# Performance work log

Hardware: AMD Instinct MI355X
Metric: run time of the kernel (lower is better)

Reference implementation:

```python
import jax, jax.numpy as jnp
import numpy as np

# Static configuration (matches init_kwargs)
B, C, H, W = 8, 64, 256, 256
WS = 8            # window size
HEADS = 4
DH = 16           # dim per head, HEADS*DH == C
L = WS * WS       # tokens per window
EPS_LN = 1e-5

# --- Swin relative-position index (static, numpy) ---
_coords = np.stack(np.meshgrid(np.arange(WS), np.arange(WS), indexing='ij'))  # [2,ws,ws]
_flat = _coords.reshape(2, -1)                                                # [2,L]
_rel = (_flat[:, :, None] - _flat[:, None, :]).transpose(1, 2, 0).copy()      # [L,L,2]
_rel[..., 0] += WS - 1
_rel[..., 1] += WS - 1
_rel[..., 0] *= 2 * WS - 1
REL_IDX = _rel.sum(-1)  # [L,L] ints in [0, (2ws-1)^2)


def _biasfree_ln(x, w):
    # x: [B,C,H,W]; BiasFree_LayerNorm over channel dim (biased var, no mean subtraction in scale)
    var = jnp.var(x, axis=1, keepdims=True)
    return x * jax.lax.rsqrt(var + EPS_LN) * w[None, :, None, None]


def _win_partition(t):  # [B,H,W,C] -> [N, L, C]
    t = t.reshape(B, H // WS, WS, W // WS, WS, C).transpose(0, 1, 3, 2, 4, 5)
    return t.reshape(-1, L, C)


def _win_reverse(t):  # [N, L, C] -> [B,H,W,C]
    t = t.reshape(B, H // WS, W // WS, WS, WS, C).transpose(0, 1, 3, 2, 4, 5)
    return t.reshape(B, H, W, C)


def _l2norm(t):
    # torch F.normalize(dim=-1) semantics
    n = jnp.sqrt(jnp.sum(t * t, axis=-1, keepdims=True))
    return t / jnp.maximum(n, 1e-12)


def _forward(x, illu_fea, ln1_w, ln2_w, w_qkv, b_qkv, rpb_table, w_proj, b_proj,
             temperature, w_qkv_m, w_dw, w_out_m):
    # ---------- spatial (window) attention branch ----------
    xs = _biasfree_ln(x, ln1_w).transpose(0, 2, 3, 1)          # [B,H,W,C]
    xw = _win_partition(xs)                                     # [N,L,C]
    iw = _win_partition(illu_fea.transpose(0, 2, 3, 1))         # [N,L,C]
    iw = iw.reshape(-1, L, HEADS, DH).transpose(0, 2, 1, 3)     # [N,h,L,d]

    qkv = (xw @ w_qkv + b_qkv).reshape(-1, L, 3, HEADS, DH).transpose(2, 0, 3, 1, 4)
    q, k, v = qkv[0], qkv[1], qkv[2]                            # [N,h,L,d]
    scale = DH ** (-0.5)
    attn = jnp.einsum('nhld,nhmd->nhlm', q * scale, k)          # [N,h,L,L]
    bias = rpb_table[REL_IDX.reshape(-1)].reshape(L, L, HEADS).transpose(2, 0, 1)
    attn = jax.nn.softmax(attn + bias[None], axis=-1)
    v = v * iw                                                  # illumination modulation
    out = jnp.einsum('nhlm,nhmd->nhld', attn, v)
    out = out.transpose(0, 2, 1, 3).reshape(-1, L, C) @ w_proj + b_proj
    win_out = _win_reverse(out).transpose(0, 3, 1, 2)           # [B,C,H,W]

    # ---------- channel (MDTA) attention branch ----------
    xm = _biasfree_ln(x, ln2_w)
    qkv_m = jnp.einsum('oc,bchw->bohw', w_qkv_m, xm)            # 1x1 conv, [B,3C,H,W]
    qkv_m = jax.lax.conv_general_dilated(
        qkv_m, w_dw, (1, 1), 'SAME', feature_group_count=3 * C,
        dimension_numbers=('NCHW', 'OIHW', 'NCHW'))             # depthwise 3x3
    qm, km, vm = jnp.split(qkv_m, 3, axis=1)                    # [B,C,H,W] each

    def heads(t):
        return t.reshape(B, HEADS, DH, H * W)                   # b (n d) h w -> b n d (hw)
    qm, km, vm, im = heads(qm), heads(km), heads(vm), heads(illu_fea)
    qm = _l2norm(qm)
    km = _l2norm(km)
    attn_c = jnp.einsum('bndx,bnex->bnde', qm, km) * temperature[None]  # [B,h,d,d]
    attn_c = jax.nn.softmax(attn_c, axis=-1)
    vm = vm * im                                                # illumination modulation
    out_c = jnp.einsum('bnde,bnex->bndx', attn_c, vm).reshape(B, C, H, W)
    mdta_out = jnp.einsum('oc,bchw->bohw', w_out_m, out_c)

    return x + win_out + mdta_out


def setup_inputs() -> dict:
    key = jax.random.key(0)
    ks = jax.random.split(key, 10)
    f32 = jnp.float32
    return {
        'x': jax.random.normal(ks[0], (B, C, H, W), f32),
        'illu_fea': jax.random.uniform(ks[1], (B, C, H, W), f32),
        'ln1_w': jnp.ones((C,), f32),
        'ln2_w': jnp.ones((C,), f32),
        'w_qkv': jax.random.normal(ks[2], (C, 3 * C), f32) * 0.02,
        'b_qkv': jnp.zeros((3 * C,), f32),
        'rpb_table': jax.random.normal(ks[3], ((2 * WS - 1) ** 2, HEADS), f32) * 0.02,
        'w_proj': jax.random.normal(ks[4], (C, C), f32) * 0.02,
        'b_proj': jnp.zeros((C,), f32),
        'temperature': jnp.ones((HEADS, 1, 1), f32),
        'w_qkv_m': jax.random.normal(ks[5], (3 * C, C), f32) * 0.02,
        'w_dw': jax.random.normal(ks[6], (3 * C, 1, 3, 3), f32) * 0.1,
        'w_out_m': jax.random.normal(ks[7], (C, C), f32) * 0.02,
    }


def reference(x, illu_fea, ln1_w, ln2_w, w_qkv, b_qkv, rpb_table, w_proj, b_proj,
              temperature, w_qkv_m, w_dw, w_out_m):
    return _forward(x, illu_fea, ln1_w, ln2_w, w_qkv, b_qkv, rpb_table, w_proj,
                    b_proj, temperature, w_qkv_m, w_dw, w_out_m)
```

## Files before the change

kernel.cpp:

```cpp
#include <hip/hip_runtime.h>
#include <hip/hip_bf16.h>

#define HW 65536
#define WIDTH 256
#define SP_OFF 77856768ull

typedef __attribute__((ext_vector_type(8))) short short8v;
typedef __attribute__((ext_vector_type(4))) short short4v;
typedef __attribute__((ext_vector_type(4))) float f32x4;

__device__ inline float bf2f(unsigned short u) {
  unsigned int i = ((unsigned int)u) << 16;
  float f; __builtin_memcpy(&f, &i, 4); return f;
}
__device__ inline unsigned short f2bf(float x) {
  __hip_bfloat16 h = __float2bfloat16(x);
  unsigned short u; __builtin_memcpy(&u, &h, 2); return u;
}

#define XH_IDX(p, g) ((p)*64 + ((((g) ^ ((p)&7)))<<3))
#define QC_IDX(ch, px) ((ch)*256 + ((((px)>>3) ^ ((ch)&7))<<3) + ((px)&7))
#define QCG_IDX(ch, G) ((ch)*256 + ((((G) ^ ((ch)&7)))<<3))

__global__ __launch_bounds__(256, 3) void k_spatial(
    const float* __restrict__ x, const float* __restrict__ illu,
    const float* __restrict__ ln1w, const float* __restrict__ wqkv,
    const float* __restrict__ bqkv, const float* __restrict__ rpb,
    const float* __restrict__ wproj, const float* __restrict__ bproj,
    float* __restrict__ out, unsigned short* __restrict__ sp, int use_sp)
{
  __shared__ __align__(16) unsigned short shbuf[9216];
  __shared__ __align__(16) unsigned short ks[64*72];
  __shared__ __align__(16) unsigned short vs[64*72];
  __shared__ __align__(16) unsigned short vsT[64*72];
  __shared__ float rpbs[900];
  __shared__ float rs_tok[64];

  unsigned short* xw = shbuf;
  unsigned short* qs = shbuf + 4608;

  const int tid = threadIdx.x;
  const int b = blockIdx.x & 7;
  const int grp = blockIdx.x >> 3;
  const float* xb = x + (size_t)b * 64 * HW;
  const float* ib = illu + (size_t)b * 64 * HW;

  const int lane = tid & 63;
  const int w = tid >> 6;
  const int fr = lane & 15;
  const int fg = lane >> 4;
  const int hb = w * 16;

  for (int i = tid; i < 900; i += 256) rpbs[i] = rpb[i];

  short8v bfq[3][2];
  float biasr[3];
  #pragma unroll
  for (int part = 0; part < 3; ++part) {
    int o = part * 64 + hb + fr;
    biasr[part] = bqkv[o];
    #pragma unroll
    for (int kh = 0; kh < 2; ++kh)
      #pragma unroll
      for (int j = 0; j < 8; ++j) {
        int c = kh * 32 + fg * 8 + j;
        bfq[part][kh][j] = (short)f2bf(wqkv[c * 192 + o] * ln1w[c]);
      }
  }
  short8v bfp[2];
  #pragma unroll
  for (int kh = 0; kh < 2; ++kh)
    #pragma unroll
    for (int j = 0; j < 8; ++j) {
      int c = kh * 32 + fg * 8 + j;
      bfp[kh][j] = (short)f2bf(wproj[c * 64 + hb + fr]);
    }

  for (int wi = 0; wi < 4; ++wi) {
    const int win = (grp << 2) + wi;
    const int h0 = (win >> 5) << 3;
    const int w0 = (win & 31) << 3;

    for (int i = tid; i < 1024; i += 256) {
      int c = i >> 4, seg = i & 15;
      int row = seg >> 1, half = (seg & 1) * 4;
      float4 v4 = *(const float4*)&xb[(size_t)c * HW + (h0 + row) * WIDTH + w0 + half];
      int p = row * 8 + half;
      xw[(p+0)*72 + c] = f2bf(v4.x);
      xw[(p+1)*72 + c] = f2bf(v4.y);
      xw[(p+2)*72 + c] = f2bf(v4.z);
      xw[(p+3)*72 + c] = f2bf(v4.w);
    }
    __syncthreads();
    {
      int l = tid >> 2, q4 = tid & 3;
      short8v v8a = *(const short8v*)&xw[l*72 + q4*16];
      short8v v8b = *(const short8v*)&xw[l*72 + q4*16 + 8];
      float s = 0.f, s2 = 0.f;
      #pragma unroll
      for (int j = 0; j < 8; ++j) {
        float va = bf2f((unsigned short)v8a[j]), vb = bf2f((unsigned short)v8b[j]);
        s += va + vb; s2 += va * va + vb * vb;
      }
      s += __shfl_down(s, 1); s2 += __shfl_down(s2, 1);
      s += __shfl_down(s, 2); s2 += __shfl_down(s2, 2);
      if (q4 == 0) {
        float mean = s * 0.015625f;
        float var = s2 * 0.015625f - mean * mean;
        rs_tok[l] = rsqrtf(var + 1e-5f);
      }
    }
    __syncthreads();
    {
      short8v a[4][2];
      #pragma unroll
      for (int rt = 0; rt < 4; ++rt)
        #pragma unroll
        for (int kh = 0; kh < 2; ++kh)
          a[rt][kh] = *(const short8v*)&xw[(rt*16 + fr)*72 + kh*32 + fg*8];
      #pragma unroll
      for (int part = 0; part < 3; ++part) {
        float bias = biasr[part];
        #pragma unroll
        for (int rt = 0; rt < 4; ++rt) {
          f32x4 acc = {0.f, 0.f, 0.f, 0.f};
          acc = __builtin_amdgcn_mfma_f32_16x16x32_bf16(a[rt][0], bfq[part][0], acc, 0, 0, 0);
          acc = __builtin_amdgcn_mfma_f32_16x16x32_bf16(a[rt][1], bfq[part][1], acc, 0, 0, 0);
          #pragma unroll
          for (int r = 0; r < 4; ++r) {
            int t = rt*16 + fg*4 + r;
            float val = acc[r] * rs_tok[t] + bias;
            if (part == 0)      qs[t*72 + hb + fr] = f2bf(val * 0.25f);
            else if (part == 1) ks[t*72 + hb + fr] = f2bf(val);
            else                vs[t*72 + hb + fr] = f2bf(val);
          }
        }
      }
    }
    __syncthreads();
    for (int i = tid; i < 1024; i += 256) {
      int c = i >> 4, seg = i & 15;
      int row = seg >> 1, half = (seg & 1) * 4;
      float4 v4 = *(const float4*)&ib[(size_t)c * HW + (h0 + row) * WIDTH + w0 + half];
      int p = row * 8 + half;
      xw[(p+0)*72 + c] = f2bf(v4.x);
      xw[(p+1)*72 + c] = f2bf(v4.y);
      xw[(p+2)*72 + c] = f2bf(v4.z);
      xw[(p+3)*72 + c] = f2bf(v4.w);
    }
    __syncthreads();
    for (int i = tid; i < 4096; i += 256) {
      int l = i >> 6, c = i & 63;
      unsigned short vb16 = f2bf(bf2f(vs[l*72 + c]) * bf2f(xw[l*72 + c]));
      vs[l*72 + c] = vb16;
      vsT[c*72 + ((((l >> 3) ^ (c & 7)) << 3) | (l & 7))] = vb16;
    }
    __syncthreads();
    float inv_s[4];
    {
      short8v zero8 = {0,0,0,0,0,0,0,0};
      short8v kf[4], qf[4];
      #pragma unroll
      for (int t = 0; t < 4; ++t) {
        if (fg < 2) {
          kf[t] = *(const short8v*)&ks[(t*16 + fr)*72 + hb + fg*8];
          qf[t] = *(const short8v*)&qs[(t*16 + fr)*72 + hb + fg*8];
        } else { kf[t] = zero8; qf[t] = zero8; }
      }
      f32x4 st[4][4];
      #pragma unroll
      for (int kt = 0; kt < 4; ++kt)
        #pragma unroll
        for (int qt = 0; qt < 4; ++qt) {
          f32x4 z = {0.f, 0.f, 0.f, 0.f};
          st[kt][qt] = __builtin_amdgcn_mfma_f32_16x16x32_bf16(kf[kt], qf[qt], z, 0, 0, 0);
        }
      float sc[4][16];
      #pragma unroll
      for (int qt = 0; qt < 4; ++qt) {
        int qi = qt*2 + (fr >> 3);
        int qj = fr & 7;
        float mx = -1e30f;
        #pragma unroll
        for (int kt = 0; kt < 4; ++kt) {
          int ki = kt*2 + (fg >> 1);
          int kj0 = (fg & 1) * 4;
          int base = ((qi - ki + 7)*15 + (qj - kj0 + 7))*4 + w;
          #pragma unroll
          for (int r = 0; r < 4; ++r) {
            float v = st[kt][qt][r] + rpbs[base - 4*r];
            sc[qt][kt*4 + r] = v;
            mx = fmaxf(mx, v);
          }
        }
        mx = fmaxf(mx, __shfl_xor(mx, 16));
        mx = fmaxf(mx, __shfl_xor(mx, 32));
        float ss = 0.f;
        #pragma unroll
        for (int j = 0; j < 16; ++j) { float e = __expf(sc[qt][j] - mx); sc[qt][j] = e; ss += e; }
        ss += __shfl_xor(ss, 16);
        ss += __shfl_xor(ss, 32);
        inv_s[qt] = 1.f / ss;
      }
      __syncthreads();
      unsigned short* pb = shbuf + w * 2304;
      f32x4 ot[4];
      #pragma unroll
      for (int nt = 0; nt < 4; ++nt) { f32x4 z = {0.f,0.f,0.f,0.f}; ot[nt] = z; }
      #pragma unroll
      for (int P = 0; P < 2; ++P) {
        #pragma unroll
        for (int qt = 0; qt < 4; ++qt)
          #pragma unroll
          for (int k2 = 0; k2 < 2; ++k2) {
            int kt = 2*P + k2;
            unsigned int lo = (unsigned)f2bf(sc[qt][kt*4+0]) | ((unsigned)f2bf(sc[qt][kt*4+1]) << 16);
            unsigned int hi = (unsigned)f2bf(sc[qt][kt*4+2]) | ((unsigned)f2bf(sc[qt][kt*4+3]) << 16);
            uint2 pk; pk.x = lo; pk.y = hi;
            *(uint2*)&pb[(qt*16 + fr)*36 + k2*16 + fg*4] = pk;
          }
        __syncthreads();
        short8v av = *(const short8v*)&vsT[(hb + fr)*72 + (((P*4 + fg) ^ ((hb + fr) & 7)) << 3)];
        #pragma unroll
        for (int nt = 0; nt < 4; ++nt) {
          short4v p0 = *(const short4v*)&pb[(nt*16 + fr)*36 + fg*8];
          short4v p1 = *(const short4v*)&pb[(nt*16 + fr)*36 + fg*8 + 4];
          short8v bv;
          #pragma unroll
          for (int j = 0; j < 4; ++j) { bv[j] = p0[j]; bv[4+j] = p1[j]; }
          ot[nt] = __builtin_amdgcn_mfma_f32_16x16x32_bf16(av, bv, ot[nt], 0, 0, 0);
        }
        __syncthreads();
      }
      #pragma unroll
      for (int nt = 0; nt < 4; ++nt) {
        float iv = inv_s[nt];
        unsigned int lo = (unsigned)f2bf(ot[nt][0]*iv) | ((unsigned)f2bf(ot[nt][1]*iv) << 16);
        unsigned int hi = (unsigned)f2bf(ot[nt][2]*iv) | ((unsigned)f2bf(ot[nt][3]*iv) << 16);
        uint2 pk; pk.x = lo; pk.y = hi;
        *(uint2*)&ks[(nt*16 + fr)*72 + hb + fg*4] = pk;
      }
    }
    __syncthreads();
    {
      short8v a[4][2];
      #pragma unroll
      for (int rt = 0; rt < 4; ++rt)
        #pragma unroll
        for (int kh = 0; kh < 2; ++kh)
          a[rt][kh] = *(const short8v*)&ks[(rt*16 + fr)*72 + kh*32 + fg*8];
      #pragma unroll
      for (int rt = 0; rt < 4; ++rt) {
        f32x4 acc = {0.f, 0.f, 0.f, 0.f};
        acc = __builtin_amdgcn_mfma_f32_16x16x32_bf16(a[rt][0], bfp[0], acc, 0, 0, 0);
        acc = __builtin_amdgcn_mfma_f32_16x16x32_bf16(a[rt][1], bfp[1], acc, 0, 0, 0);
        #pragma unroll
        for (int r = 0; r < 4; ++r)
          vs[(rt*16 + fg*4 + r)*72 + hb + fr] = f2bf(acc[r]);
      }
    }
    __syncthreads();
    if (use_sp) {
      unsigned short* spw = sp + (size_t)(b * 1024 + win) * 4096;
      for (int i = tid; i < 1024; i += 256) {
        int row = i >> 7, rem = i & 127;
        int c = rem >> 1, half = (rem & 1) * 4;
        int p = row * 8 + half;
        size_t gofs = (size_t)c * HW + (h0 + row) * WIDTH + w0 + half;
        float4 xr4 = *(const float4*)&xb[gofs];
        float bp = bproj[c];
        unsigned int lo = (unsigned)f2bf(xr4.x + bp + bf2f(vs[(p+0)*72 + c]))
                        | ((unsigned)f2bf(xr4.y + bp + bf2f(vs[(p+1)*72 + c])) << 16);
        unsigned int hi = (unsigned)f2bf(xr4.z + bp + bf2f(vs[(p+2)*72 + c]))
                        | ((unsigned)f2bf(xr4.w + bp + bf2f(vs[(p+3)*72 + c])) << 16);
        uint2 pk; pk.x = lo; pk.y = hi;
        *(uint2*)&spw[row*512 + c*8 + half] = pk;
      }
    } else {
      for (int i = tid; i < 1024; i += 256) {
        int o = i >> 4, seg = i & 15;
        int row = seg >> 1, half = (seg & 1) * 4;
        int p = row * 8 + half;
        size_t gofs = (size_t)o * HW + (h0 + row) * WIDTH + w0 + half;
        float4 xr4 = *(const float4*)&xb[gofs];
        float bp = bproj[o];
        float4 r;
        r.x = xr4.x + bp + bf2f(vs[(p+0)*72 + o]);
        r.y = xr4.y + bp + bf2f(vs[(p+1)*72 + o]);
        r.z = xr4.z + bp + bf2f(vs[(p+2)*72 + o]);
        r.w = xr4.w + bp + bf2f(vs[(p+3)*72 + o]);
        *(float4*)&out[(size_t)b * 64 * HW + gofs] = r;
      }
    }
    __syncthreads();
  }
}

__global__ __launch_bounds__(256, 2) void k_chan_qkv(
    const float* __restrict__ x, const float* __restrict__ illu,
    const float* __restrict__ ln2w, const float* __restrict__ w1,
    const float* __restrict__ wdw,
    unsigned short* __restrict__ vm, float* __restrict__ Gp,
    float* __restrict__ Nqp, float* __restrict__ Nkp)
{
  __shared__ __align__(16) unsigned short xh[324*64];
  __shared__ __align__(16) unsigned short tb[32*360];
  __shared__ __align__(16) unsigned short qc[16*256];
  __shared__ __align__(16) unsigned short kc[16*256];

  float* rsp = (float*)tb;

  const int tid = threadIdx.x;
  const int blk = blockIdx.x;
  const int b = blk >> 8;
  const int tile = blk & 255;
  const int ty0 = (tile >> 4) << 4, tx0 = (tile & 15) << 4;
  const float* xb = x + (size_t)b * 64 * HW;

  for (int i = tid; i < 64 * 324; i += 256) {
    int c = i / 324, p = i - c * 324;
    int hy = p / 18, hx = p - hy * 18;
    int gy = ty0 + hy - 1, gx = tx0 + hx - 1;
    float v = 0.f;
    if (gy >= 0 && gy < 256 && gx >= 0 && gx < 256)
      v = xb[(size_t)c * HW + gy * WIDTH + gx];
    xh[XH_IDX(p, c >> 3) + (c & 7)] = f2bf(v);
  }
  __syncthreads();
  for (int p = tid; p < 324; p += 256) {
    float s = 0.f, s2 = 0.f;
    #pragma unroll
    for (int g = 0; g < 8; ++g) {
      short8v v8 = *(const short8v*)&xh[XH_IDX(p, g)];
      #pragma unroll
      for (int j = 0; j < 8; ++j) { float v = bf2f((unsigned short)v8[j]); s += v; s2 += v * v; }
    }
    float mean = s * 0.015625f;
    float var = s2 * 0.015625f - mean * mean;
    rsp[p] = rsqrtf(var + 1e-5f);
  }
  __syncthreads();
  for (int i = tid; i < 2592; i += 256) {
    int p = i >> 3;
    float rs = rsp[p];
    short8v v8 = *(const short8v*)&xh[i * 8];
    #pragma unroll
    for (int j = 0; j < 8; ++j) v8[j] = (short)f2bf(bf2f((unsigned short)v8[j]) * rs);
    *(short8v*)&xh[i * 8] = v8;
  }
  __syncthreads();

  const int lane = tid & 63;
  const int wid = tid >> 6;
  const int fcol = lane & 15;
  const int fk = lane >> 4;
  const int dpy = (tid >> 2) & 15;
  const int dg = tid & 3;

  auto gemm32 = [&](int qb, int kb) {
    short8v bq[2], bk[2];
    const float* wrq = w1 + (size_t)(qb + fcol) * 64;
    const float* wrk = w1 + (size_t)(kb + fcol) * 64;
    #pragma unroll
    for (int s = 0; s < 2; ++s) {
      int cs = fk * 8 + s * 32;
      #pragma unroll
      for (int j = 0; j < 8; ++j) {
        float lw = ln2w[cs + j];
        bq[s][j] = (short)f2bf(wrq[cs + j] * lw);
        bk[s][j] = (short)f2bf(wrk[cs + j] * lw);
      }
    }
    for (int t = wid; t < 21; t += 4) {
      int ar = t * 16 + fcol;
      short8v a0 = *(const short8v*)&xh[XH_IDX(ar, fk)];
      short8v a1 = *(const short8v*)&xh[XH_IDX(ar, fk + 4)];
      f32x4 aq = {0.f, 0.f, 0.f, 0.f};
      f32x4 ak = {0.f, 0.f, 0.f, 0.f};
      aq = __builtin_amdgcn_mfma_f32_16x16x32_bf16(a0, bq[0], aq, 0, 0, 0);
      aq = __builtin_amdgcn_mfma_f32_16x16x32_bf16(a1, bq[1], aq, 0, 0, 0);
      ak = __builtin_amdgcn_mfma_f32_16x16x32_bf16(a0, bk[0], ak, 0, 0, 0);
      ak = __builtin_amdgcn_mfma_f32_16x16x32_bf16(a1, bk[1], ak, 0, 0, 0);
      #pragma unroll
      for (int r = 0; r < 4; ++r) {
        int px = t * 16 + fk * 4 + r;
        if (px < 324) {
          int hy = px / 18, hx = px - hy * 18;
          tb[fcol * 360 + hy * 20 + hx]        = f2bf(aq[r]);
          tb[(16 + fcol) * 360 + hy * 20 + hx] = f2bf(ak[r]);
        }
      }
    }
  };

  float dout8[8][4];
  auto dw32 = [&](int qwb, int kwb) {
    #pragma unroll
    for (int oc8 = 0; oc8 < 8; ++oc8) {
      int oc = wid * 8 + oc8;
      int ch = (oc < 16) ? (qwb + oc) : (kwb + oc - 16);
      const float* w9 = wdw + (size_t)ch * 9;
      float wk[9];
      #pragma unroll
      for (int t = 0; t < 9; ++t) wk[t] = w9[t];
      float a0 = 0.f, a1 = 0.f, a2 = 0.f, a3 = 0.f;
      #pragma unroll
      for (int ky = 0; ky < 3; ++ky) {
        int base = oc * 360 + (dpy + ky) * 20 + dg * 4;
        short4v t4 = *(const short4v*)&tb[base];
        unsigned int t2 = *(const unsigned int*)&tb[base + 4];
        float e0 = bf2f((unsigned short)t4[0]);
        float e1 = bf2f((unsigned short)t4[1]);
        float e2 = bf2f((unsigned short)t4[2]);
        float e3 = bf2f((unsigned short)t4[3]);
        float e4 = bf2f((unsigned short)(t2 & 0xffff));
        float e5 = bf2f((unsigned short)(t2 >> 16));
        float k0 = wk[ky*3+0], k1 = wk[ky*3+1], k2 = wk[ky*3+2];
        a0 += k0*e0 + k1*e1 + k2*e2;
        a1 += k0*e1 + k1*e2 + k2*e3;
        a2 += k0*e2 + k1*e3 + k2*e4;
        a3 += k0*e3 + k1*e4 + k2*e5;
      }
      dout8[oc8][0] = a0; dout8[oc8][1] = a1;
      dout8[oc8][2] = a2; dout8[oc8][3] = a3;
    }
  };

  for (int n = 0; n < 4; ++n) {
    gemm32(16 * n, 64 + 16 * n);
    __syncthreads();
    dw32(16 * n, 64 + 16 * n);
    #pragma unroll
    for (int oc8 = 0; oc8 < 8; ++oc8) {
      int oc = wid * 8 + oc8;
      unsigned short* dst = (oc < 16) ? qc : kc;
      int row = oc & 15;
      #pragma unroll
      for (int i = 0; i < 4; ++i)
        dst[QC_IDX(row, dpy*16 + dg*4 + i)] = f2bf(dout8[oc8][i]);
    }
    __syncthreads();
    {
      int ch = tid >> 4, seg = tid & 15;
      float sq = 0.f, sk = 0.f;
      #pragma unroll
      for (int j = 0; j < 16; ++j) {
        float vq = bf2f(qc[QC_IDX(ch, seg * 16 + j)]); sq += vq * vq;
        float vk = bf2f(kc[QC_IDX(ch, seg * 16 + j)]); sk += vk * vk;
      }
      sq += __shfl_xor(sq, 1); sq += __shfl_xor(sq, 2); sq += __shfl_xor(sq, 4); sq += __shfl_xor(sq, 8);
      sk += __shfl_xor(sk, 1); sk += __shfl_xor(sk, 2); sk += __shfl_xor(sk, 4); sk += __shfl_xor(sk, 8);
      if (seg == 0) {
        Nqp[(size_t)blk * 64 + n * 16 + ch] = sq;
        Nkp[(size_t)blk * 64 + n * 16 + ch] = sk;
      }
    }
    if (wid == 0) {
      f32x4 g = {0.f, 0.f, 0.f, 0.f};
      #pragma unroll
      for (int s = 0; s < 8; ++s) {
        int G = fk + 4 * s;
        short8v aq = *(const short8v*)&qc[QCG_IDX(fcol, G)];
        short8v bk = *(const short8v*)&kc[QCG_IDX(fcol, G)];
        g = __builtin_amdgcn_mfma_f32_16x16x32_bf16(aq, bk, g, 0, 0, 0);
      }
      float* gp = Gp + ((size_t)blk * 4 + n) * 256;
      #pragma unroll
      for (int r = 0; r < 4; ++r) gp[(fk * 4 + r) * 16 + fcol] = g[r];
    }
  }
  const float* ib = illu + (size_t)b * 64 * HW;
  for (int j = 0; j < 2; ++j) {
    gemm32(128 + 32 * j, 144 + 32 * j);
    __syncthreads();
    dw32(128 + 32 * j, 144 + 32 * j);
    int gy = ty0 + dpy, gx = tx0 + dg * 4;
    size_t ppos = (size_t)gy * WIDTH + gx;
    #pragma unroll
    for (int oc8 = 0; oc8 < 8; ++oc8) {
      int vc = 32 * j + wid * 8 + oc8;
      float4 iv4 = *(const float4*)&ib[(size_t)vc * HW + ppos];
      unsigned int lo = (unsigned)f2bf(dout8[oc8][0] * iv4.x)
                      | ((unsigned)f2bf(dout8[oc8][1] * iv4.y) << 16);
      unsigned int hi = (unsigned)f2bf(dout8[oc8][2] * iv4.z)
                      | ((unsigned)f2bf(dout8[oc8][3] * iv4.w) << 16);
      uint2 pk; pk.x = lo; pk.y = hi;
      *(uint2*)&vm[((size_t)b * 64 + vc) * HW + ppos] = pk;
    }
    __syncthreads();
  }
}

__global__ __launch_bounds__(256) void k_reduce1(
    const float* __restrict__ Gp, const float* __restrict__ Nqp, const float* __restrict__ Nkp,
    float* __restrict__ G2, float* __restrict__ Nq2, float* __restrict__ Nk2)
{
  const int blk = blockIdx.x;
  const int b = blk >> 5, g = blk & 31;
  const int tid = threadIdx.x;
  float ga[4] = {0.f, 0.f, 0.f, 0.f};
  for (int t = 0; t < 8; ++t) {
    const float* src = Gp + ((size_t)(b * 256 + g * 8 + t)) * 1024;
    #pragma unroll
    for (int j = 0; j < 4; ++j) ga[j] += src[tid + j * 256];
  }
  float* dst = G2 + ((size_t)(b * 32 + g)) * 1024;
  #pragma unroll
  for (int j = 0; j < 4; ++j) dst[tid + j * 256] = ga[j];
  if (tid < 128) {
    int ch = tid & 63; bool isq = tid < 64;
    const float* np = isq ? Nqp : Nkp;
    float s = 0.f;
    for (int t = 0; t < 8; ++t) s += np[((size_t)(b * 256 + g * 8 + t)) * 64 + ch];
    (isq ? Nq2 : Nk2)[(size_t)(b * 32 + g) * 64 + ch] = s;
  }
}

__global__ __launch_bounds__(256) void k_reduce2(
    const float* __restrict__ G2, const float* __restrict__ Nq2, const float* __restrict__ Nk2,
    const float* __restrict__ temp, const float* __restrict__ wout, float* __restrict__ M)
{
  __shared__ float Gs[1024];
  __shared__ float As[4][16][17];
  __shared__ float nq[64], nk[64];
  const int b = blockIdx.x;
  const int tid = threadIdx.x;
  float ga[4] = {0.f, 0.f, 0.f, 0.f};
  for (int g = 0; g < 32; ++g) {
    const float* src = G2 + ((size_t)(b * 32 + g)) * 1024;
    #pragma unroll
    for (int j = 0; j < 4; ++j) ga[j] += src[tid + j * 256];
  }
  #pragma unroll
  for (int j = 0; j < 4; ++j) Gs[tid + j * 256] = ga[j];
  if (tid < 128) {
    int ch = tid & 63; bool isq = tid < 64;
    const float* n2 = isq ? Nq2 : Nk2;
    float s = 0.f;
    for (int g = 0; g < 32; ++g) s += n2[(size_t)(b * 32 + g) * 64 + ch];
    float r = fmaxf(sqrtf(s), 1e-12f);
    (isq ? nq : nk)[ch] = r;
  }
  __syncthreads();
  if (tid < 64) {
    int n = tid >> 4, d = tid & 15;
    float tv = temp[n];
    float row[16]; float mx = -1e30f;
    #pragma unroll
    for (int e = 0; e < 16; ++e) {
      float v = Gs[n * 256 + d * 16 + e] / (nq[n * 16 + d] * nk[n * 16 + e]) * tv;
      row[e] = v; mx = fmaxf(mx, v);
    }
    float s = 0.f;
    #pragma unroll
    for (int e = 0; e < 16; ++e) { float ev = __expf(row[e] - mx); row[e] = ev; s += ev; }
    float inv = 1.f / s;
    #pragma unroll
    for (int e = 0; e < 16; ++e) As[n][d][e] = row[e] * inv;
  }
  __syncthreads();
  float* Mb = M + (size_t)b * 4096;
  for (int i = tid; i < 4096; i += 256) {
    int o = i >> 6, cp = i & 63;
    int n = cp >> 4, e = cp & 15;
    float a = 0.f;
    #pragma unroll
    for (int d = 0; d < 16; ++d) a += wout[o * 64 + n * 16 + d] * As[n][d][e];
    Mb[i] = a;
  }
}

__global__ __launch_bounds__(256, 3) void k_mdta_out(
    const unsigned short* __restrict__ vm, const float* __restrict__ M,
    const unsigned short* __restrict__ sp, int use_sp,
    float* __restrict__ out)
{
  __shared__ __align__(16) float Ml[4096];
  __shared__ __align__(16) unsigned short spl[64 * 264];
  const int blk = blockIdx.x;
  const int b = blk >> 8;
  const int y = blk & 255;
  const int tid = threadIdx.x;

  const float* Mb = M + (size_t)b * 4096;
  for (int i = tid; i < 4096; i += 256) Ml[i] = Mb[i];
  if (use_sp) {
    int wy = y >> 3, py = y & 7;
    const unsigned short* spb = sp + ((((size_t)b * 1024 + wy * 32) * 8) + py) * 512;
    for (int k = 0; k < 8; ++k) {
      int i3 = k * 256 + tid;
      int o = i3 & 63, wx = i3 >> 6;
      short8v v8 = *(const short8v*)&spb[(size_t)wx * 4096 + o * 8];
      *(short8v*)&spl[o * 264 + wx * 8] = v8;
    }
  }
  __syncthreads();
  float xcol[64];
  const unsigned short* vb = vm + (size_t)b * 64 * HW + y * 256 + tid;
  #pragma unroll
  for (int c = 0; c < 64; ++c) xcol[c] = bf2f(vb[(size_t)c * HW]);
  float* ob = out + (size_t)b * 64 * HW + y * 256 + tid;
  for (int o = 0; o < 64; ++o) {
    const float4* mr = (const float4*)&Ml[o * 64];
    float acc = 0.f;
    #pragma unroll
    for (int g = 0; g < 16; ++g) {
      float4 m4 = mr[g];
      acc += m4.x * xcol[g*4] + m4.y * xcol[g*4+1] + m4.z * xcol[g*4+2] + m4.w * xcol[g*4+3];
    }
    if (use_sp) ob[(size_t)o * HW] = bf2f(spl[o * 264 + tid]) + acc;
    else        ob[(size_t)o * HW] += acc;
  }
}

extern "C" void kernel_launch(void* const* d_in, const int* in_sizes, int n_in,
                              void* d_out, int out_size, void* d_ws, size_t ws_size,
                              hipStream_t stream) {
  const float* x     = (const float*)d_in[0];
  const float* illu  = (const float*)d_in[1];
  const float* ln1w  = (const float*)d_in[2];
  const float* ln2w  = (const float*)d_in[3];
  const float* wqkv  = (const float*)d_in[4];
  const float* bqkv  = (const float*)d_in[5];
  const float* rpb   = (const float*)d_in[6];
  const float* wproj = (const float*)d_in[7];
  const float* bproj = (const float*)d_in[8];
  const float* temp  = (const float*)d_in[9];
  const float* w1    = (const float*)d_in[10];
  const float* wdw   = (const float*)d_in[11];
  const float* wout  = (const float*)d_in[12];
  float* out = (float*)d_out;

  char* ws = (char*)d_ws;
  unsigned short* vm = (unsigned short*)ws;
  float* Gp  = (float*)(ws + 67108864);
  float* Nqp = (float*)(ws + 75497472);
  float* Nkp = (float*)(ws + 76021760);
  float* G2  = (float*)(ws + 76546048);
  float* Nq2 = (float*)(ws + 77594624);
  float* Nk2 = (float*)(ws + 77660160);
  float* M   = (float*)(ws + 77725696);
  unsigned short* sp = (unsigned short*)(ws + SP_OFF);
  int use_sp = (ws_size >= SP_OFF + 67108864ull) ? 1 : 0;

  k_spatial<<<2048, 256, 0, stream>>>(x, illu, ln1w, wqkv, bqkv, rpb, wproj, bproj,
                                      out, sp, use_sp);
  k_chan_qkv<<<2048, 256, 0, stream>>>(x, illu, ln2w, w1, wdw, vm, Gp, Nqp, Nkp);
  k_reduce1<<<256, 256, 0, stream>>>(Gp, Nqp, Nkp, G2, Nq2, Nk2);
  k_reduce2<<<8, 256, 0, stream>>>(G2, Nq2, Nk2, temp, wout, M);
  k_mdta_out<<<2048, 256, 0, stream>>>(vm, M, sp, use_sp, out);
}
```

Before: 728.0 us.

## Switch channel-branch QKV projection to FP8 MFMA and shrink shared memory

The k_chan_qkv kernel now stores the normalized input halo tile in FP8 e4m3 instead of bf16 and runs the pointwise QKV projection with fp8 MFMA instructions. The weights are pre-scaled by 64 and the outputs are scaled back. The q/k staging buffers are aliased onto the depthwise-conv buffer, with extra barriers added, so the LDS footprint drops and launch bounds rise to 3 blocks per SM for higher occupancy. The cost is reduced precision in the projection and LayerNorm statistics, which risks tolerance failures, plus extra synchronization.

```diff
diff --git a/kernel.cpp b/kernel.cpp
--- a/kernel.cpp
+++ b/kernel.cpp
@@ -1,5 +1,6 @@
 #include <hip/hip_runtime.h>
 #include <hip/hip_bf16.h>
+#include <hip/hip_fp8.h>
 
 #define HW 65536
 #define WIDTH 256
@@ -17,8 +18,17 @@
   __hip_bfloat16 h = __float2bfloat16(x);
   unsigned short u; __builtin_memcpy(&u, &h, 2); return u;
 }
-
-#define XH_IDX(p, g) ((p)*64 + ((((g) ^ ((p)&7)))<<3))
+__device__ inline unsigned char f2fp8(float x) {
+  __hip_fp8_e4m3 h(x);
+  unsigned char u; __builtin_memcpy(&u, &h.__x, 1); return u;
+}
+__device__ inline float fp82f(unsigned char u) {
+  __hip_fp8_e4m3 h;
+  __builtin_memcpy(&h.__x, &u, 1);
+  return (float)h;
+}
+
+#define XH8(p, g) ((p)*64 + (((((g) + ((p)>>1))) & 7) << 3))
 #define QC_IDX(ch, px) ((ch)*256 + ((((px)>>3) ^ ((ch)&7))<<3) + ((px)&7))
 #define QCG_IDX(ch, G) ((ch)*256 + ((((G) ^ ((ch)&7)))<<3))
 
@@ -296,18 +306,18 @@
   }
 }
 
-__global__ __launch_bounds__(256, 2) void k_chan_qkv(
+__global__ __launch_bounds__(256, 3) void k_chan_qkv(
     const float* __restrict__ x, const float* __restrict__ illu,
     const float* __restrict__ ln2w, const float* __restrict__ w1,
     const float* __restrict__ wdw,
     unsigned short* __restrict__ vm, float* __restrict__ Gp,
     float* __restrict__ Nqp, float* __restrict__ Nkp)
 {
-  __shared__ __align__(16) unsigned short xh[324*64];
-  __shared__ __align__(16) unsigned short tb[32*360];
-  __shared__ __align__(16) unsigned short qc[16*256];
-  __shared__ __align__(16) unsigned short kc[16*256];
-
+  __shared__ __align__(16) unsigned char xh[336*64];
+  __shared__ __align__(16) unsigned short tb[32*504];
+
+  unsigned short* qc = tb;
+  unsigned short* kc = tb + 4096;
   float* rsp = (float*)tb;
 
   const int tid = threadIdx.x;
@@ -324,16 +334,23 @@
     float v = 0.f;
     if (gy >= 0 && gy < 256 && gx >= 0 && gx < 256)
       v = xb[(size_t)c * HW + gy * WIDTH + gx];
-    xh[XH_IDX(p, c >> 3) + (c & 7)] = f2bf(v);
+    xh[XH8(p, c >> 3) + (c & 7)] = f2fp8(v);
+  }
+  for (int i = tid; i < 12 * 64; i += 256) {
+    int p = 324 + (i >> 6), c = i & 63;
+    xh[XH8(p, c >> 3) + (c & 7)] = 0;
   }
   __syncthreads();
   for (int p = tid; p < 324; p += 256) {
     float s = 0.f, s2 = 0.f;
     #pragma unroll
     for (int g = 0; g < 8; ++g) {
-      short8v v8 = *(const short8v*)&xh[XH_IDX(p, g)];
-      #pragma unroll
-      for (int j = 0; j < 8; ++j) { float v = bf2f((unsigned short)v8[j]); s += v; s2 += v * v; }
+      unsigned long long v8 = *(const unsigned long long*)&xh[XH8(p, g)];
+      #pragma unroll
+      for (int j = 0; j < 8; ++j) {
+        float v = fp82f((unsigned char)(v8 >> (8*j)));
+        s += v; s2 += v * v;
+      }
     }
     float mean = s * 0.015625f;
     float var = s2 * 0.015625f - mean * mean;
@@ -341,12 +358,17 @@
   }
   __syncthreads();
   for (int i = tid; i < 2592; i += 256) {
-    int p = i >> 3;
+    int p = i >> 3, g = i & 7;
     float rs = rsp[p];
-    short8v v8 = *(const short8v*)&xh[i * 8];
-    #pragma unroll
-    for (int j = 0; j < 8; ++j) v8[j] = (short)f2bf(bf2f((unsigned short)v8[j]) * rs);
-    *(short8v*)&xh[i * 8] = v8;
+    unsigned char* a = &xh[XH8(p, g)];
+    unsigned long long v8 = *(const unsigned long long*)a;
+    unsigned long long o8 = 0;
+    #pragma unroll
+    for (int j = 0; j < 8; ++j) {
+      float v = fp82f((unsigned char)(v8 >> (8*j))) * rs;
+      o8 |= ((unsigned long long)f2fp8(v)) << (8*j);
+    }
+    *(unsigned long long*)a = o8;
   }
   __syncthreads();
 
@@ -358,36 +380,39 @@
   const int dg = tid & 3;
 
   auto gemm32 = [&](int qb, int kb) {
-    short8v bq[2], bk[2];
+    long long bq[2], bk[2];
     const float* wrq = w1 + (size_t)(qb + fcol) * 64;
     const float* wrk = w1 + (size_t)(kb + fcol) * 64;
     #pragma unroll
     for (int s = 0; s < 2; ++s) {
       int cs = fk * 8 + s * 32;
+      unsigned char tq[8], tk[8];
       #pragma unroll
       for (int j = 0; j < 8; ++j) {
-        float lw = ln2w[cs + j];
-        bq[s][j] = (short)f2bf(wrq[cs + j] * lw);
-        bk[s][j] = (short)f2bf(wrk[cs + j] * lw);
-      }
+        float lw = ln2w[cs + j] * 64.f;
+        tq[j] = f2fp8(wrq[cs + j] * lw);
+        tk[j] = f2fp8(wrk[cs + j] * lw);
+      }
+      __builtin_memcpy(&bq[s], tq, 8);
+      __builtin_memcpy(&bk[s], tk, 8);
     }
     for (int t = wid; t < 21; t += 4) {
       int ar = t * 16 + fcol;
-      short8v a0 = *(const short8v*)&xh[XH_IDX(ar, fk)];
-      short8v a1 = *(const short8v*)&xh[XH_IDX(ar, fk + 4)];
+      long long a0 = *(const long long*)&xh[XH8(ar, fk)];
+      long long a1 = *(const long long*)&xh[XH8(ar, fk + 4)];
       f32x4 aq = {0.f, 0.f, 0.f, 0.f};
       f32x4 ak = {0.f, 0.f, 0.f, 0.f};
-      aq = __builtin_amdgcn_mfma_f32_16x16x32_bf16(a0, bq[0], aq, 0, 0, 0);
-      aq = __builtin_amdgcn_mfma_f32_16x16x32_bf16(a1, bq[1], aq, 0, 0, 0);
-      ak = __builtin_amdgcn_mfma_f32_16x16x32_bf16(a0, bk[0], ak, 0, 0, 0);
-      ak = __builtin_amdgcn_mfma_f32_16x16x32_bf16(a1, bk[1], ak, 0, 0, 0);
+      aq = __builtin_amdgcn_mfma_f32_16x16x32_fp8_fp8(a0, bq[0], aq, 0, 0, 0);
+      aq = __builtin_amdgcn_mfma_f32_16x16x32_fp8_fp8(a1, bq[1], aq, 0, 0, 0);
+      ak = __builtin_amdgcn_mfma_f32_16x16x32_fp8_fp8(a0, bk[0], ak, 0, 0, 0);
+      ak = __builtin_amdgcn_mfma_f32_16x16x32_fp8_fp8(a1, bk[1], ak, 0, 0, 0);
       #pragma unroll
       for (int r = 0; r < 4; ++r) {
         int px = t * 16 + fk * 4 + r;
         if (px < 324) {
           int hy = px / 18, hx = px - hy * 18;
-          tb[fcol * 360 + hy * 20 + hx]        = f2bf(aq[r]);
-          tb[(16 + fcol) * 360 + hy * 20 + hx] = f2bf(ak[r]);
+          tb[fcol * 504 + hy * 28 + hx]        = f2bf(aq[r] * 0.015625f);
+          tb[(16 + fcol) * 504 + hy * 28 + hx] = f2bf(ak[r] * 0.015625f);
         }
       }
     }
@@ -406,7 +431,7 @@
       float a0 = 0.f, a1 = 0.f, a2 = 0.f, a3 = 0.f;
       #pragma unroll
       for (int ky = 0; ky < 3; ++ky) {
-        int base = oc * 360 + (dpy + ky) * 20 + dg * 4;
+        int base = oc * 504 + (dpy + ky) * 28 + dg * 4;
         short4v t4 = *(const short4v*)&tb[base];
         unsigned int t2 = *(const unsigned int*)&tb[base + 4];
         float e0 = bf2f((unsigned short)t4[0]);
@@ -430,6 +455,7 @@
     gemm32(16 * n, 64 + 16 * n);
     __syncthreads();
     dw32(16 * n, 64 + 16 * n);
+    __syncthreads();
     #pragma unroll
     for (int oc8 = 0; oc8 < 8; ++oc8) {
       int oc = wid * 8 + oc8;
@@ -468,6 +494,7 @@
       #pragma unroll
       for (int r = 0; r < 4; ++r) gp[(fk * 4 + r) * 16 + fcol] = g[r];
     }
+    __syncthreads();
   }
   const float* ib = illu + (size_t)b * 64 * HW;
   for (int j = 0; j < 2; ++j) {
```

Result: slower. 768.0 us (+5.5%).
